# Kernel tuning notes

Measured on AMD Instinct MI355X. Metric: run time of the kernel, lower is better.

## Reference

```python
import jax, jax.numpy as jnp
import numpy as np

IN_DIM = 65 * 9 + 2  # 587
HIDDEN = [256, 256, 256, 256]
OUT_DIM = 3


def _unfold3(feat):
    # F.unfold(feat, 3, padding=1).view(B, C*9, h, w): channel order (c, ki, kj)
    B, C, h, w = feat.shape
    p = jnp.pad(feat, ((0, 0), (0, 0), (1, 1), (1, 1)))
    patches = jnp.stack(
        [p[:, :, ki:ki + h, kj:kj + w] for ki in range(3) for kj in range(3)],
        axis=2,
    )  # [B, C, 9, h, w]
    return patches.reshape(B, C * 9, h, w)


def _mlp(x, Ws, bs):
    for i, (W, b) in enumerate(zip(Ws, bs)):
        x = x @ W + b
        if i < len(Ws) - 1:
            x = jax.nn.relu(x)
    return x


def setup_inputs() -> dict:
    key = jax.random.key(0)
    ks = jax.random.split(key, 16)
    B, Cf, h, w = 1, 64, 128, 128
    H, W = 256, 256
    inp = {
        'masked_feat': jax.random.normal(ks[0], (B, Cf, h, w), jnp.float32),
        'mask': (jax.random.uniform(ks[1], (B, 1, h, w)) > 0.5).astype(jnp.float32),
        'gt_feat': jax.random.normal(ks[2], (B, 3, H, W), jnp.float32),
        'hr_coord': jax.random.uniform(ks[3], (B, H * W, 2), jnp.float32, minval=-1.0, maxval=1.0),
    }
    dims = [IN_DIM] + HIDDEN + [OUT_DIM]
    for i in range(len(dims) - 1):
        scale = 1.0 / np.sqrt(dims[i])
        inp[f'W{i}'] = jax.random.uniform(ks[4 + 2 * i], (dims[i], dims[i + 1]), jnp.float32, minval=-scale, maxval=scale)
        inp[f'b{i}'] = jax.random.uniform(ks[5 + 2 * i], (dims[i + 1],), jnp.float32, minval=-scale, maxval=scale)
    return inp


def _liif(feat, coord, Ws, bs):
    B, Cu, h, w = feat.shape
    Q = coord.shape[1]
    featf = feat.reshape(B, Cu, h * w)
    rx = 1.0 / h  # 2/h/2
    ry = 1.0 / w
    eps_shift = 1e-6
    preds, areas = [], []
    for vx in (-1, 1):
        for vy in (-1, 1):
            cy = jnp.clip(coord[:, :, 0] + vx * rx + eps_shift, -1 + 1e-6, 1 - 1e-6)
            cx = jnp.clip(coord[:, :, 1] + vy * ry + eps_shift, -1 + 1e-6, 1 - 1e-6)
            # grid_sample nearest, align_corners=False: pix = ((c+1)*size - 1)/2
            iy = jnp.clip(jnp.round(((cy + 1.0) * h - 1.0) * 0.5).astype(jnp.int32), 0, h - 1)
            ix = jnp.clip(jnp.round(((cx + 1.0) * w - 1.0) * 0.5).astype(jnp.int32), 0, w - 1)
            idx = iy * w + ix  # [B, Q]
            q_feat = jnp.take_along_axis(featf, idx[:, None, :], axis=2)  # [B, Cu, Q]
            q_feat = jnp.transpose(q_feat, (0, 2, 1))  # [B, Q, Cu]
            # feat_coord (make_coord cell centers) sampled at same nearest index
            qy = -1.0 + (2.0 * iy.astype(coord.dtype) + 1.0) / h
            qx = -1.0 + (2.0 * ix.astype(coord.dtype) + 1.0) / w
            rel0 = (coord[:, :, 0] - qy) * h
            rel1 = (coord[:, :, 1] - qx) * w
            inp = jnp.concatenate([q_feat, rel0[..., None], rel1[..., None]], axis=-1)
            pred = _mlp(inp.reshape(B * Q, -1), Ws, bs).reshape(B, Q, -1)
            preds.append(pred)
            areas.append(jnp.abs(rel0 * rel1) + 1e-9)
    tot_area = areas[0] + areas[1] + areas[2] + areas[3]
    # local_ensemble: swap 0<->3, 1<->2 (diagonal weighting)
    areas = [areas[3], areas[2], areas[1], areas[0]]
    ret = 0
    for pred, area in zip(preds, areas):
        ret = ret + pred * (area / tot_area)[..., None]
    return ret  # [B, Q, out_dim]


def reference(masked_feat, mask, gt_feat, hr_coord,
              W0, b0, W1, b1, W2, b2, W3, b3, W4, b4):
    Ws = [W0, W1, W2, W3, W4]
    bs = [b0, b1, b2, b3, b4]
    feat = jnp.concatenate([masked_feat, mask], axis=1)  # [B, 65, h, w]
    feat = _unfold3(feat)  # [B, 585, h, w]
    out = _liif(feat, hr_coord, Ws, bs)  # [B, Q, 3]
    B, _, H, W = gt_feat.shape
    out = jnp.transpose(out.reshape(B, H, W, -1), (0, 3, 1, 2))  # [B, 3, H, W]
    return out
```

## Files before the change

kernel.cpp:

```cpp
#include <hip/hip_runtime.h>

typedef _Float16 f16;
typedef _Float16 half8 __attribute__((ext_vector_type(8)));
typedef float f32x4 __attribute__((ext_vector_type(4)));

#define NTHREADS 512
#define HSTR 264
#define XSTR 616

#define WP_TOTAL_HALFS 356352
#define U_OFF_BYTES 712704

__device__ __forceinline__ void gload_lds16(const void* g, void* l) {
    __builtin_amdgcn_global_load_lds(
        (const __attribute__((address_space(1))) unsigned int*)g,
        (__attribute__((address_space(3))) unsigned int*)l, 16, 0, 0);
}

__device__ __forceinline__ void stage_chunk(const char* src, void* dst, int nbytes, int wv, int ln) {
    for (int off = wv * 1024; off < nbytes; off += 8192)
        gload_lds16(src + off + (ln << 4), (char*)dst + off);
}

__global__ void prep_weights(const float* __restrict__ W0, const float* __restrict__ W1,
                             const float* __restrict__ W2, const float* __restrict__ W3,
                             const float* __restrict__ W4, f16* __restrict__ wp) {
    int idx = blockIdx.x * 256 + threadIdx.x;
    if (idx >= WP_TOTAL_HALFS) return;
    float v = 0.f;
    if (idx < 155648) {
        int k0 = idx >> 11;
        int rem = idx & 2047;
        int n = rem >> 3, j = rem & 7;
        int k = k0 * 8 + j;
        if (k < 587) v = W0[k * 256 + n];
    } else if (idx < 352256) {
        int local = idx - 155648;
        int l = local >> 16;
        int ll = local & 65535;
        int k0 = ll >> 11;
        int rem = ll & 2047;
        int n = rem >> 3, j = rem & 7;
        int k = k0 * 8 + j;
        const float* W = (l == 0) ? W1 : (l == 1) ? W2 : W3;
        v = W[k * 256 + n];
    } else {
        int local = idx - 352256;
        int k0 = local >> 7;
        int rem = local & 127;
        int n = rem >> 3, j = rem & 7;
        int k = k0 * 8 + j;
        if (n < 3) v = W4[k * 3 + n];
    }
    wp[idx] = (f16)v;
}

__global__ __launch_bounds__(NTHREADS, 2)
void u_gemm(const float* __restrict__ feat, const float* __restrict__ mask,
            const float* __restrict__ b0, const f16* __restrict__ wp,
            f16* __restrict__ U) {
    __shared__ __align__(16) f16 sX[64 * XSTR];
    __shared__ __align__(16) f16 sW[2][8192];

    const int tid = threadIdx.x;
    const int wv  = tid >> 6;
    const int ln  = tid & 63;
    const int lo  = ln & 15;
    const int hi  = ln >> 4;

    const int cell0 = blockIdx.x * 64;
    const int y  = cell0 >> 7;
    const int x0 = cell0 & 127;

    stage_chunk((const char*)wp, &sW[0][0], 16384, wv, ln);

    {
        int r = tid & 63;
        int part = tid >> 6;
        #pragma unroll
        for (int o = 0; o < 9; ++o) {
            int ki = o / 3, kj = o % 3;
            int yy = y + ki - 1;
            int xx = x0 + r + kj - 1;
            bool ok = ((unsigned)yy < 128u) && ((unsigned)xx < 128u);
            for (int c = part; c < 65; c += 8) {
                float v = 0.f;
                if (ok) v = (c < 64) ? feat[(c << 14) + (yy << 7) + xx] : mask[(yy << 7) + xx];
                sX[r * XSTR + c * 9 + o] = (f16)v;
            }
        }
    }
    if (tid < 64) {
        for (int k = 585; k < 608; ++k) sX[tid * XSTR + k] = (f16)0.f;
    }
    __syncthreads();

    f32x4 acc[4][2];
    #pragma unroll
    for (int m = 0; m < 4; ++m) { acc[m][0] = f32x4{0,0,0,0}; acc[m][1] = f32x4{0,0,0,0}; }

    for (int g = 0; g < 19; ++g) {
        if (g + 1 < 19)
            stage_chunk((const char*)wp + (g + 1) * 16384, &sW[(g + 1) & 1][0], 16384, wv, ln);
        const f16* wbuf = &sW[g & 1][0];
        half8 a[4], b[2];
        #pragma unroll
        for (int t = 0; t < 2; ++t)
            b[t] = *(const half8*)&wbuf[hi * 2048 + ((wv * 2 + t) * 16 + lo) * 8];
        #pragma unroll
        for (int m = 0; m < 4; ++m)
            a[m] = *(const half8*)&sX[(m * 16 + lo) * XSTR + g * 32 + hi * 8];
        #pragma unroll
        for (int m = 0; m < 4; ++m) {
            #pragma unroll
            for (int t = 0; t < 2; ++t)
                acc[m][t] = __builtin_amdgcn_mfma_f32_16x16x32_f16(a[m], b[t], acc[m][t], 0, 0, 0);
        }
        __syncthreads();
    }

    #pragma unroll
    for (int t = 0; t < 2; ++t) {
        int n = (wv * 2 + t) * 16 + lo;
        float bv = b0[n];
        #pragma unroll
        for (int m = 0; m < 4; ++m) {
            #pragma unroll
            for (int i = 0; i < 4; ++i) {
                int cell = cell0 + m * 16 + hi * 4 + i;
                U[cell * 256 + n] = (f16)(acc[m][t][i] + bv);
            }
        }
    }
}

__global__ __launch_bounds__(NTHREADS, 4)
void liif_main(const float* __restrict__ coord, const float* __restrict__ W0,
               const float* __restrict__ b1, const float* __restrict__ b2,
               const float* __restrict__ b3, const float* __restrict__ b4,
               const f16* __restrict__ wp, const f16* __restrict__ U,
               float* __restrict__ out) {
    __shared__ __align__(16) f16 sAct[64 * HSTR];
    __shared__ __align__(16) f16 sW[2][8192];
    __shared__ float sRel0[64], sRel1[64], sArea[64];
    __shared__ int   sCell[64];
    __shared__ float sPred[64 * 4];

    const int tid = threadIdx.x;
    const int wv  = tid >> 6;
    const int ln  = tid & 63;
    const int lo  = ln & 15;
    const int hi  = ln >> 4;

    const char* wbase = (const char*)wp + 311296;

    stage_chunk(wbase, &sW[0][0], 16384, wv, ln);

    if (tid < 64) {
        int r = tid;
        int R = blockIdx.x * 64 + r;
        int q = R >> 2, s = R & 3;
        float c0 = coord[q * 2 + 0];
        float c1 = coord[q * 2 + 1];
        float vx = (s & 2) ? 1.0f : -1.0f;
        float vy = (s & 1) ? 1.0f : -1.0f;
        const float rxy = 0.0078125f;
        const float LOC = (float)(-1.0 + 1e-6);
        const float HIC = (float)( 1.0 - 1e-6);
        float cy = fminf(fmaxf(c0 + vx * rxy + 1e-6f, LOC), HIC);
        float cx = fminf(fmaxf(c1 + vy * rxy + 1e-6f, LOC), HIC);
        int iy = (int)rintf(((cy + 1.0f) * 128.0f - 1.0f) * 0.5f);
        int ix = (int)rintf(((cx + 1.0f) * 128.0f - 1.0f) * 0.5f);
        iy = min(max(iy, 0), 127);
        ix = min(max(ix, 0), 127);
        float qy = -1.0f + ((float)(2 * iy) + 1.0f) * rxy;
        float qx = -1.0f + ((float)(2 * ix) + 1.0f) * rxy;
        float rel0 = (c0 - qy) * 128.0f;
        float rel1 = (c1 - qx) * 128.0f;
        sCell[r] = iy * 128 + ix;
        sRel0[r] = rel0;
        sRel1[r] = rel1;
        sArea[r] = fabsf(rel0 * rel1) + 1e-9f;
    }
    __syncthreads();

    {
        int r = tid >> 3, j = tid & 7;
        int cell = sCell[r];
        float r0 = sRel0[r], r1 = sRel1[r];
        const f16* ub = U + cell * 256 + j * 32;
        const float* wa = W0 + 585 * 256 + j * 32;
        const float* wb = W0 + 586 * 256 + j * 32;
        #pragma unroll
        for (int q = 0; q < 4; ++q) {
            half8 u = *(const half8*)(ub + q * 8);
            half8 hv;
            #pragma unroll
            for (int e = 0; e < 8; ++e) {
                float h = (float)u[e] + r0 * wa[q * 8 + e] + r1 * wb[q * 8 + e];
                hv[e] = (f16)fmaxf(h, 0.f);
            }
            *(half8*)&sAct[r * HSTR + j * 32 + q * 8] = hv;
        }
    }
    __syncthreads();

    f32x4 acc[4][2];
    #pragma unroll
    for (int m = 0; m < 4; ++m) { acc[m][0] = f32x4{0,0,0,0}; acc[m][1] = f32x4{0,0,0,0}; }

    for (int g = 0; g <= 24; ++g) {
        if (g < 24) {
            int nc = g + 1;
            stage_chunk(wbase + nc * 16384, &sW[nc & 1][0], (nc == 24) ? 8192 : 16384, wv, ln);
        }

        if (g < 24) {
            const f16* wbuf = &sW[g & 1][0];
            int ks = g & 7;
            half8 a[4], b[2];
            #pragma unroll
            for (int t = 0; t < 2; ++t)
                b[t] = *(const half8*)&wbuf[hi * 2048 + ((wv * 2 + t) * 16 + lo) * 8];
            #pragma unroll
            for (int m = 0; m < 4; ++m)
                a[m] = *(const half8*)&sAct[(m * 16 + lo) * HSTR + ks * 32 + hi * 8];
            #pragma unroll
            for (int m = 0; m < 4; ++m) {
                #pragma unroll
                for (int t = 0; t < 2; ++t)
                    acc[m][t] = __builtin_amdgcn_mfma_f32_16x16x32_f16(a[m], b[t], acc[m][t], 0, 0, 0);
            }
        } else if (wv < 4) {
            const f16* wbuf = &sW[0][0];
            #pragma unroll
            for (int ks = 0; ks < 8; ++ks) {
                half8 bf = *(const half8*)&wbuf[(ks * 4 + hi) * 128 + lo * 8];
                half8 a  = *(const half8*)&sAct[(wv * 16 + lo) * HSTR + ks * 32 + hi * 8];
                acc[0][0] = __builtin_amdgcn_mfma_f32_16x16x32_f16(a, bf, acc[0][0], 0, 0, 0);
            }
        }
        __syncthreads();

        if (g == 7 || g == 15 || g == 23) {
            const float* bias = (g == 7) ? b1 : (g == 15) ? b2 : b3;
            #pragma unroll
            for (int t = 0; t < 2; ++t) {
                int n = (wv * 2 + t) * 16 + lo;
                float bv = bias[n];
                #pragma unroll
                for (int m = 0; m < 4; ++m) {
                    #pragma unroll
                    for (int i = 0; i < 4; ++i) {
                        int r = m * 16 + hi * 4 + i;
                        sAct[r * HSTR + n] = (f16)fmaxf(acc[m][t][i] + bv, 0.f);
                    }
                    acc[m][t] = f32x4{0,0,0,0};
                }
            }
            __syncthreads();
        }
    }

    if (wv < 4 && lo < 4) {
        float bv = (lo < 3) ? b4[lo] : 0.f;
        #pragma unroll
        for (int i = 0; i < 4; ++i) {
            int r = wv * 16 + hi * 4 + i;
            sPred[r * 4 + lo] = acc[0][0][i] + bv;
        }
    }
    __syncthreads();

    if (tid < 48) {
        int qloc = tid / 3;
        int ch = tid - qloc * 3;
        int rb = qloc * 4;
        float a0 = sArea[rb + 0], a1 = sArea[rb + 1], a2 = sArea[rb + 2], a3 = sArea[rb + 3];
        float tot = a0 + a1 + a2 + a3;
        float v = sPred[(rb + 0) * 4 + ch] * (a3 / tot)
                + sPred[(rb + 1) * 4 + ch] * (a2 / tot)
                + sPred[(rb + 2) * 4 + ch] * (a1 / tot)
                + sPred[(rb + 3) * 4 + ch] * (a0 / tot);
        out[ch * 65536 + blockIdx.x * 16 + qloc] = v;
    }
}

extern "C" void kernel_launch(void* const* d_in, const int* in_sizes, int n_in,
                              void* d_out, int out_size, void* d_ws, size_t ws_size,
                              hipStream_t stream) {
    const float* feat  = (const float*)d_in[0];
    const float* mask  = (const float*)d_in[1];
    const float* coord = (const float*)d_in[3];
    const float* W0 = (const float*)d_in[4];
    const float* b0 = (const float*)d_in[5];
    const float* W1 = (const float*)d_in[6];
    const float* b1 = (const float*)d_in[7];
    const float* W2 = (const float*)d_in[8];
    const float* b2 = (const float*)d_in[9];
    const float* W3 = (const float*)d_in[10];
    const float* b3 = (const float*)d_in[11];
    const float* W4 = (const float*)d_in[12];
    const float* b4 = (const float*)d_in[13];
    f16* wp = (f16*)d_ws;
    f16* U  = (f16*)((char*)d_ws + U_OFF_BYTES);
    float* outp = (float*)d_out;

    prep_weights<<<(WP_TOTAL_HALFS + 255) / 256, 256, 0, stream>>>(W0, W1, W2, W3, W4, wp);
    u_gemm<<<256, NTHREADS, 0, stream>>>(feat, mask, b0, wp, U);
    liif_main<<<4096, NTHREADS, 0, stream>>>(coord, W0, b1, b2, b3, b4, wp, U, outp);
}
```

Measured before the change: 333.4 us.

## Stream MLP weights from global into registers, double 128-row tiles, swizzle LDS activations

The hidden-layer GEMMs no longer stage weight chunks into LDS. Each wave now loads its weight fragments directly from global/L2 into registers, double-buffered across K steps, and computes a 64x64 output tile (4x4 MFMAs) instead of 64x32. Each block processes 128 rows rather than 64, so there are half as many blocks. The activation buffer is unpadded with an XOR swizzle to avoid LDS bank conflicts, and the weight pre-pack layout is changed to match the new fragment loads. This removes the LDS staging traffic and the per-chunk barriers, at the cost of higher register pressure and reliance on L2 for weight reads, which may reduce occupancy.

Measured after the change: 307.3 us. -7.8%, faster.

```diff
diff --git a/kernel.cpp b/kernel.cpp
--- a/kernel.cpp
+++ b/kernel.cpp
@@ -2,13 +2,15 @@
 
 typedef _Float16 f16;
 typedef _Float16 half8 __attribute__((ext_vector_type(8)));
+typedef _Float16 half4 __attribute__((ext_vector_type(4)));
 typedef float f32x4 __attribute__((ext_vector_type(4)));
 
 #define NTHREADS 512
-#define HSTR 264
 #define XSTR 616
 
 #define WP_TOTAL_HALFS 356352
+#define WT_OFF_H   155648
+#define W4_OFF_H   352256
 #define U_OFF_BYTES 712704
 
 __device__ __forceinline__ void gload_lds16(const void* g, void* l) {
@@ -28,29 +30,26 @@
     int idx = blockIdx.x * 256 + threadIdx.x;
     if (idx >= WP_TOTAL_HALFS) return;
     float v = 0.f;
-    if (idx < 155648) {
+    if (idx < WT_OFF_H) {
         int k0 = idx >> 11;
         int rem = idx & 2047;
         int n = rem >> 3, j = rem & 7;
         int k = k0 * 8 + j;
         if (k < 587) v = W0[k * 256 + n];
-    } else if (idx < 352256) {
-        int local = idx - 155648;
-        int l = local >> 16;
-        int ll = local & 65535;
-        int k0 = ll >> 11;
-        int rem = ll & 2047;
-        int n = rem >> 3, j = rem & 7;
-        int k = k0 * 8 + j;
+    } else if (idx < W4_OFF_H) {
+        int local = idx - WT_OFF_H;
+        int kk = local & 31;
+        int rowi = local >> 5;
+        int n = rowi & 255;
+        int lc = rowi >> 8;
+        int l = lc >> 3, c = lc & 7;
+        int k = c * 32 + kk;
         const float* W = (l == 0) ? W1 : (l == 1) ? W2 : W3;
         v = W[k * 256 + n];
     } else {
-        int local = idx - 352256;
-        int k0 = local >> 7;
-        int rem = local & 127;
-        int n = rem >> 3, j = rem & 7;
-        int k = k0 * 8 + j;
-        if (n < 3) v = W4[k * 3 + n];
+        int local = idx - W4_OFF_H;
+        int n = local >> 8, k = local & 255;
+        v = (n < 3) ? W4[k * 3 + n] : 0.f;
     }
     wp[idx] = (f16)v;
 }
@@ -140,25 +139,22 @@
                const float* __restrict__ b3, const float* __restrict__ b4,
                const f16* __restrict__ wp, const f16* __restrict__ U,
                float* __restrict__ out) {
-    __shared__ __align__(16) f16 sAct[64 * HSTR];
-    __shared__ __align__(16) f16 sW[2][8192];
-    __shared__ float sRel0[64], sRel1[64], sArea[64];
-    __shared__ int   sCell[64];
-    __shared__ float sPred[64 * 4];
+    __shared__ __align__(16) f16 sAct[128 * 256];
+    __shared__ float sRel0[128], sRel1[128], sArea[128];
+    __shared__ int   sCell[128];
+    __shared__ float sPred[128 * 4];
 
     const int tid = threadIdx.x;
     const int wv  = tid >> 6;
     const int ln  = tid & 63;
     const int lo  = ln & 15;
     const int hi  = ln >> 4;
-
-    const char* wbase = (const char*)wp + 311296;
-
-    stage_chunk(wbase, &sW[0][0], 16384, wv, ln);
-
-    if (tid < 64) {
+    const int ng  = wv & 3;
+    const int qg  = wv >> 2;
+
+    if (tid < 128) {
         int r = tid;
-        int R = blockIdx.x * 64 + r;
+        int R = blockIdx.x * 128 + r;
         int q = R >> 2, s = R & 3;
         float c0 = coord[q * 2 + 0];
         float c1 = coord[q * 2 + 1];
@@ -185,104 +181,123 @@
     __syncthreads();
 
     {
-        int r = tid >> 3, j = tid & 7;
-        int cell = sCell[r];
-        float r0 = sRel0[r], r1 = sRel1[r];
-        const f16* ub = U + cell * 256 + j * 32;
-        const float* wa = W0 + 585 * 256 + j * 32;
-        const float* wb = W0 + 586 * 256 + j * 32;
-        #pragma unroll
-        for (int q = 0; q < 4; ++q) {
-            half8 u = *(const half8*)(ub + q * 8);
+        int row = tid >> 2, p = tid & 3;
+        int cell = sCell[row];
+        float r0 = sRel0[row], r1 = sRel1[row];
+        const half8* up = (const half8*)(U + cell * 256 + p * 64);
+        const float* wa = W0 + 585 * 256 + p * 64;
+        const float* wb = W0 + 586 * 256 + p * 64;
+        char* rowbase = (char*)sAct + row * 512;
+        int swz = (row & 7) << 4;
+        #pragma unroll
+        for (int e = 0; e < 8; ++e) {
+            half8 u = up[e];
             half8 hv;
             #pragma unroll
-            for (int e = 0; e < 8; ++e) {
-                float h = (float)u[e] + r0 * wa[q * 8 + e] + r1 * wb[q * 8 + e];
-                hv[e] = (f16)fmaxf(h, 0.f);
+            for (int j = 0; j < 8; ++j) {
+                float h = (float)u[j] + r0 * wa[e * 8 + j] + r1 * wb[e * 8 + j];
+                hv[j] = (f16)fmaxf(h, 0.f);
             }
-            *(half8*)&sAct[r * HSTR + j * 32 + q * 8] = hv;
+            *(half8*)(rowbase + ((p * 128 + e * 16) ^ swz)) = hv;
         }
     }
     __syncthreads();
 
-    f32x4 acc[4][2];
+    const f16* wT = wp + WT_OFF_H;
+    const f16* aBase = wT + ng * 2048 + lo * 32 + hi * 8;
+    const int rowb = qg * 64 + lo;
+    const int swzb = (lo & 7) << 4;
+    const char* actb = (const char*)sAct + rowb * 512;
+
+    f32x4 acc[4][4];
     #pragma unroll
-    for (int m = 0; m < 4; ++m) { acc[m][0] = f32x4{0,0,0,0}; acc[m][1] = f32x4{0,0,0,0}; }
-
-    for (int g = 0; g <= 24; ++g) {
-        if (g < 24) {
-            int nc = g + 1;
-            stage_chunk(wbase + nc * 16384, &sW[nc & 1][0], (nc == 24) ? 8192 : 16384, wv, ln);
-        }
-
-        if (g < 24) {
-            const f16* wbuf = &sW[g & 1][0];
-            int ks = g & 7;
-            half8 a[4], b[2];
+    for (int i = 0; i < 4; ++i)
+        #pragma unroll
+        for (int j = 0; j < 4; ++j) acc[i][j] = f32x4{0,0,0,0};
+
+    #define LOADA(A, c) { \
+        const f16* p_ = aBase + (c) * 8192; \
+        A[0] = *(const half8*)(p_); \
+        A[1] = *(const half8*)(p_ + 512); \
+        A[2] = *(const half8*)(p_ + 1024); \
+        A[3] = *(const half8*)(p_ + 1536); }
+
+    #define LOADB(B, g) { \
+        int byte_ = ((((g) & 7) * 4 + hi) << 4) ^ swzb; \
+        B[0] = *(const half8*)(actb + byte_); \
+        B[1] = *(const half8*)(actb + 8192 + byte_); \
+        B[2] = *(const half8*)(actb + 16384 + byte_); \
+        B[3] = *(const half8*)(actb + 24576 + byte_); }
+
+    #define MF(A, B) { \
+        _Pragma("unroll") \
+        for (int ni = 0; ni < 4; ++ni) { \
+            _Pragma("unroll") \
+            for (int qj = 0; qj < 4; ++qj) \
+                acc[ni][qj] = __builtin_amdgcn_mfma_f32_16x16x32_f16(A[ni], B[qj], acc[ni][qj], 0, 0, 0); } }
+
+    #define EPI(bias) { \
+        __syncthreads(); \
+        _Pragma("unroll") \
+        for (int ni = 0; ni < 4; ++ni) { \
+            int nb_ = ng * 64 + ni * 16 + hi * 4; \
+            f32x4 bv_ = *(const f32x4*)((bias) + nb_); \
+            _Pragma("unroll") \
+            for (int qj = 0; qj < 4; ++qj) { \
+                int q_ = qg * 64 + qj * 16 + lo; \
+                half4 h_; \
+                _Pragma("unroll") \
+                for (int r = 0; r < 4; ++r) h_[r] = (f16)fmaxf(acc[ni][qj][r] + bv_[r], 0.f); \
+                *(half4*)((char*)sAct + q_ * 512 + ((nb_ * 2) ^ ((q_ & 7) << 4))) = h_; \
+                acc[ni][qj] = f32x4{0,0,0,0}; \
+            } } \
+        __syncthreads(); }
+
+    half8 a0[4], a1[4], b[4];
+    LOADA(a0, 0);
+    for (int gg = 0; gg < 12; ++gg) {
+        int g = gg * 2;
+        LOADA(a1, g + 1);
+        LOADB(b, g);
+        MF(a0, b);
+        if (g + 2 < 24) LOADA(a0, g + 2);
+        LOADB(b, g + 1);
+        MF(a1, b);
+        if (g + 1 == 7)       EPI(b1)
+        else if (g + 1 == 15) EPI(b2)
+        else if (g + 1 == 23) EPI(b3)
+    }
+
+    {
+        f32x4 acc4 = f32x4{0,0,0,0};
+        const f16* w4 = wp + W4_OFF_H + lo * 256 + hi * 8;
+        const int row4 = wv * 16 + lo;
+        const char* act4 = (const char*)sAct + row4 * 512;
+        const int swz4 = (row4 & 7) << 4;
+        #pragma unroll
+        for (int ks = 0; ks < 8; ++ks) {
+            half8 a = *(const half8*)(w4 + ks * 32);
+            half8 bb = *(const half8*)(act4 + ((((ks * 4 + hi) << 4)) ^ swz4));
+            acc4 = __builtin_amdgcn_mfma_f32_16x16x32_f16(a, bb, acc4, 0, 0, 0);
+        }
+        if (hi == 0) {
             #pragma unroll
-            for (int t = 0; t < 2; ++t)
-                b[t] = *(const half8*)&wbuf[hi * 2048 + ((wv * 2 + t) * 16 + lo) * 8];
-            #pragma unroll
-            for (int m = 0; m < 4; ++m)
-                a[m] = *(const half8*)&sAct[(m * 16 + lo) * HSTR + ks * 32 + hi * 8];
-            #pragma unroll
-            for (int m = 0; m < 4; ++m) {
-                #pragma unroll
-                for (int t = 0; t < 2; ++t)
-                    acc[m][t] = __builtin_amdgcn_mfma_f32_16x16x32_f16(a[m], b[t], acc[m][t], 0, 0, 0);
-            }
-        } else if (wv < 4) {
-            const f16* wbuf = &sW[0][0];
-            #pragma unroll
-            for (int ks = 0; ks < 8; ++ks) {
-                half8 bf = *(const half8*)&wbuf[(ks * 4 + hi) * 128 + lo * 8];
-                half8 a  = *(const half8*)&sAct[(wv * 16 + lo) * HSTR + ks * 32 + hi * 8];
-                acc[0][0] = __builtin_amdgcn_mfma_f32_16x16x32_f16(a, bf, acc[0][0], 0, 0, 0);
-            }
-        }
-        __syncthreads();
-
-        if (g == 7 || g == 15 || g == 23) {
-            const float* bias = (g == 7) ? b1 : (g == 15) ? b2 : b3;
-            #pragma unroll
-            for (int t = 0; t < 2; ++t) {
-                int n = (wv * 2 + t) * 16 + lo;
-                float bv = bias[n];
-                #pragma unroll
-                for (int m = 0; m < 4; ++m) {
-                    #pragma unroll
-                    for (int i = 0; i < 4; ++i) {
-                        int r = m * 16 + hi * 4 + i;
-                        sAct[r * HSTR + n] = (f16)fmaxf(acc[m][t][i] + bv, 0.f);
-                    }
-                    acc[m][t] = f32x4{0,0,0,0};
-                }
-            }
-            __syncthreads();
-        }
-    }
-
-    if (wv < 4 && lo < 4) {
-        float bv = (lo < 3) ? b4[lo] : 0.f;
-        #pragma unroll
-        for (int i = 0; i < 4; ++i) {
-            int r = wv * 16 + hi * 4 + i;
-            sPred[r * 4 + lo] = acc[0][0][i] + bv;
+            for (int r = 0; r < 3; ++r) sPred[row4 * 4 + r] = acc4[r] + b4[r];
         }
     }
     __syncthreads();
 
-    if (tid < 48) {
+    if (tid < 96) {
         int qloc = tid / 3;
         int ch = tid - qloc * 3;
         int rb = qloc * 4;
-        float a0 = sArea[rb + 0], a1 = sArea[rb + 1], a2 = sArea[rb + 2], a3 = sArea[rb + 3];
-        float tot = a0 + a1 + a2 + a3;
-        float v = sPred[(rb + 0) * 4 + ch] * (a3 / tot)
-                + sPred[(rb + 1) * 4 + ch] * (a2 / tot)
-                + sPred[(rb + 2) * 4 + ch] * (a1 / tot)
-                + sPred[(rb + 3) * 4 + ch] * (a0 / tot);
-        out[ch * 65536 + blockIdx.x * 16 + qloc] = v;
+        float a0_ = sArea[rb + 0], a1_ = sArea[rb + 1], a2_ = sArea[rb + 2], a3_ = sArea[rb + 3];
+        float tot = a0_ + a1_ + a2_ + a3_;
+        float v = sPred[(rb + 0) * 4 + ch] * (a3_ / tot)
+                + sPred[(rb + 1) * 4 + ch] * (a2_ / tot)
+                + sPred[(rb + 2) * 4 + ch] * (a1_ / tot)
+                + sPred[(rb + 3) * 4 + ch] * (a0_ / tot);
+        out[ch * 65536 + blockIdx.x * 32 + qloc] = v;
     }
 }
 
@@ -308,5 +323,5 @@
 
     prep_weights<<<(WP_TOTAL_HALFS + 255) / 256, 256, 0, stream>>>(W0, W1, W2, W3, W4, wp);
     u_gemm<<<256, NTHREADS, 0, stream>>>(feat, mask, b0, wp, U);
-    liif_main<<<4096, NTHREADS, 0, stream>>>(coord, W0, b1, b2, b3, b4, wp, U, outp);
-}
+    liif_main<<<2048, NTHREADS, 0, stream>>>(coord, W0, b1, b2, b3, b4, wp, U, outp);
+}
```
